# Kernel optimization log

Hardware: AMD Instinct MI355X
Metric: run time of the kernel (lower is better)

The kernel has to match this reference:

```python
import jax, jax.numpy as jnp
import numpy as np

N_NODES = 50000
N_EDGES = 800000
D_IN = 256
D_OUT = 256
N_REL = 8


def setup_inputs() -> dict:
    key = jax.random.key(0)
    k_x, k_ei, k_et, k_w = jax.random.split(key, 4)
    x = jax.random.normal(k_x, (N_NODES, D_IN), dtype=jnp.float32)
    edge_index = jax.random.randint(k_ei, (2, N_EDGES), 0, N_NODES, dtype=jnp.int32)
    edge_type = jax.random.randint(k_et, (N_EDGES,), 0, N_REL, dtype=jnp.int32)
    # xavier_uniform-style init for per-relation weights [R, I, O]
    limit = float(np.sqrt(6.0 / (D_IN + D_OUT)))
    weight = jax.random.uniform(k_w, (N_REL, D_IN, D_OUT), dtype=jnp.float32,
                                minval=-limit, maxval=limit)
    bias = jnp.zeros((D_OUT,), dtype=jnp.float32)
    return {"x": x, "edge_index": edge_index, "edge_type": edge_type,
            "weight": weight, "bias": bias}


def reference(x, edge_index, edge_type, weight, bias):
    # RGCN (block / per-relation weights):
    #   out[row] += x[col] @ weight[edge_type]
    # Vectorized: transform every node under every relation once (dense GEMM),
    # then gather the right (relation, col) slice per edge and scatter-add to row.
    num_nodes = x.shape[0]
    row, col = edge_index[0], edge_index[1]
    xt = jnp.einsum('ni,rio->rno', x, weight)          # [R, N, O]
    messages = xt[edge_type, col]                       # [E, O]
    out = jax.ops.segment_sum(messages, row, num_segments=num_nodes)  # [N, O]
    return jax.nn.relu(out + bias)
```

## Files before the change

### kernel.cpp

```cpp
#include <hip/hip_runtime.h>
#include <hip/hip_bf16.h>
#include <stdint.h>

typedef __attribute__((ext_vector_type(8))) short short8;
typedef __attribute__((ext_vector_type(4))) float f32x4;

#define D 256
#define NTY 4

static __device__ __forceinline__ float b2f(unsigned short u) {
  union { unsigned u; float f; } c; c.u = ((unsigned)u) << 16; return c.f;
}
static __device__ __forceinline__ unsigned short f2b(float f) {
  union { float f; unsigned u; } c; c.f = f;
  unsigned r = (c.u + 0x7FFFu + ((c.u >> 16) & 1u)) >> 16;
  return (unsigned short)r;
}

static __device__ __forceinline__ void gload16(const void* g, void* l) {
  __builtin_amdgcn_global_load_lds(
      (const __attribute__((address_space(1))) unsigned int*)g,
      (__attribute__((address_space(3))) unsigned int*)l, 16, 0, 0);
}

__global__ void k_cvt_x(const float* __restrict__ x, unsigned short* __restrict__ xb,
                        long n_elems, long pad_elems) {
  long i4 = (long)blockIdx.x * 256 + threadIdx.x;
  if (i4 * 4 >= pad_elems) return;
  ushort4 o;
  if (i4 * 4 < n_elems) {
    float4 v = ((const float4*)x)[i4];
    o.x = f2b(v.x); o.y = f2b(v.y); o.z = f2b(v.z); o.w = f2b(v.w);
  } else {
    o.x = 0; o.y = 0; o.z = 0; o.w = 0;
  }
  ((ushort4*)xb)[i4] = o;
}

__global__ void k_cvt_w(const float* __restrict__ w, unsigned short* __restrict__ wt,
                        int total) {
  int t = blockIdx.x * 256 + threadIdx.x;
  if (t >= total) return;
  int i = t & 255;
  int orow = t >> 8;
  int r = orow >> 8, o = orow & 255;
  wt[t] = f2b(w[((size_t)(r * 256 + i)) * 256 + o]);
}

__global__ __launch_bounds__(256) void k_gemm(const unsigned short* __restrict__ A,
                                              const unsigned short* __restrict__ B,
                                              unsigned short* __restrict__ C,
                                              int ldc) {
  __shared__ __align__(16) char lA[64 * 512];
  __shared__ __align__(16) char lB[128 * 128];
  const int t = threadIdx.x;
  const int lane = t & 63;
  const int wave = t >> 6;
  const int l15 = lane & 15, lhi = lane >> 4;
  const size_t tm = (size_t)blockIdx.x * 64;
  const int y0 = blockIdx.y * NTY;

#pragma unroll
  for (int it = 0; it < 8; ++it) {
    int s = it * 256 + t;
    int row = s >> 5, c = s & 31;
    gload16(A + (tm + row) * 256 + ((c ^ (row & 7)) * 8),
            lA + (it * 256 + wave * 64) * 16);
  }

  for (int y = y0; y < y0 + NTY; ++y) {
    const int tn = y * 128;
    f32x4 acc[4][2];
#pragma unroll
    for (int a = 0; a < 4; ++a)
#pragma unroll
      for (int b = 0; b < 2; ++b)
#pragma unroll
        for (int e = 0; e < 4; ++e) acc[a][b][e] = 0.f;

    for (int kt = 0; kt < 256; kt += 64) {
      __syncthreads();
#pragma unroll
      for (int it = 0; it < 4; ++it) {
        int s = it * 256 + t;
        int row = s >> 3, c = s & 7;
        gload16(B + (tn + row) * 256 + kt + ((c ^ (row & 7)) * 8),
                lB + (it * 256 + wave * 64) * 16);
      }
      __syncthreads();

      short8 af[4][2], bfv[2][2];
      const int ktc = kt >> 3;
#pragma unroll
      for (int mi = 0; mi < 4; ++mi) {
#pragma unroll
        for (int kk = 0; kk < 2; ++kk) {
          int R = mi * 16 + l15;
          int c = ktc + kk * 4 + lhi;
          af[mi][kk] = *(const short8*)(lA + R * 512 + ((c ^ (R & 7)) * 16));
        }
      }
#pragma unroll
      for (int ni = 0; ni < 2; ++ni) {
#pragma unroll
        for (int kk = 0; kk < 2; ++kk) {
          int R2 = wave * 32 + ni * 16 + l15;
          int c2 = kk * 4 + lhi;
          bfv[ni][kk] = *(const short8*)(lB + R2 * 128 + ((c2 ^ (R2 & 7)) * 16));
        }
      }
#pragma unroll
      for (int mi = 0; mi < 4; ++mi) {
#pragma unroll
        for (int ni = 0; ni < 2; ++ni) {
          acc[mi][ni] = __builtin_amdgcn_mfma_f32_16x16x32_bf16(af[mi][0], bfv[ni][0], acc[mi][ni], 0, 0, 0);
          acc[mi][ni] = __builtin_amdgcn_mfma_f32_16x16x32_bf16(af[mi][1], bfv[ni][1], acc[mi][ni], 0, 0, 0);
        }
      }
    }
#pragma unroll
    for (int mi = 0; mi < 4; ++mi) {
#pragma unroll
      for (int j = 0; j < 4; ++j) {
        size_t row = tm + mi * 16 + lhi * 4 + j;
        unsigned pk = (unsigned)f2b(acc[mi][0][j]) | ((unsigned)f2b(acc[mi][1][j]) << 16);
        *(unsigned*)(C + row * (size_t)ldc + tn + wave * 32 + l15 * 2) = pk;
      }
    }
  }
}

__global__ void k_zero(int* p, int n) {
  int i = blockIdx.x * 256 + threadIdx.x;
  if (i < n) p[i] = 0;
}
__global__ void k_deg(const int* __restrict__ ei, int* deg, int E) {
  int e = blockIdx.x * 256 + threadIdx.x;
  if (e < E) atomicAdd(&deg[ei[e]], 1);
}
__global__ void k_scan1(const int* __restrict__ deg, int* bsum, int n) {
  __shared__ int sm[256];
  int t = threadIdx.x, idx = blockIdx.x * 256 + t;
  sm[t] = idx < n ? deg[idx] : 0;
  __syncthreads();
  for (int off = 128; off; off >>= 1) {
    if (t < off) sm[t] += sm[t + off];
    __syncthreads();
  }
  if (t == 0) bsum[blockIdx.x] = sm[0];
}
__global__ void k_scan2(const int* __restrict__ bsum, int* boff, int* rowptr,
                        int nsc, int Nn) {
  __shared__ int sm[256];
  int t = threadIdx.x;
  int v = t < nsc ? bsum[t] : 0;
  sm[t] = v;
  __syncthreads();
  for (int off = 1; off < 256; off <<= 1) {
    int x = t >= off ? sm[t - off] : 0;
    __syncthreads();
    sm[t] += x;
    __syncthreads();
  }
  if (t < nsc) boff[t] = sm[t] - v;
  if (t == nsc - 1) rowptr[Nn] = sm[t];
}
__global__ void k_scan3(const int* __restrict__ deg, const int* __restrict__ boff,
                        int* rowptr, int* cursor, int n) {
  __shared__ int sm[256];
  int t = threadIdx.x, idx = blockIdx.x * 256 + t;
  int v = idx < n ? deg[idx] : 0;
  sm[t] = v;
  __syncthreads();
  for (int off = 1; off < 256; off <<= 1) {
    int x = t >= off ? sm[t - off] : 0;
    __syncthreads();
    sm[t] += x;
    __syncthreads();
  }
  if (idx < n) {
    int e = boff[blockIdx.x] + sm[t] - v;
    rowptr[idx] = e;
    cursor[idx] = e;
  }
}
__global__ void k_bin(const int* __restrict__ ei, const int* __restrict__ et,
                      int* cursor, unsigned* ect, int E) {
  int e = blockIdx.x * 256 + threadIdx.x;
  if (e >= E) return;
  int r = ei[e], c = ei[E + e], ty = et[e];
  int pos = atomicAdd(&cursor[r], 1);
  ect[pos] = (unsigned)c | ((unsigned)ty << 20);
}

__global__ __launch_bounds__(256) void k_gather(const unsigned* __restrict__ ect,
                                                const int* __restrict__ rowptr,
                                                const unsigned short* __restrict__ xt,
                                                const float* __restrict__ bias,
                                                float* __restrict__ out, int n, int ldxt) {
  __shared__ float sm[4][256];
  int lane = threadIdx.x & 63;
  int wid = threadIdx.x >> 6;
  int row = blockIdx.x * 4 + wid;
  if (row >= n) return;
  int s = rowptr[row], e = rowptr[row + 1];
  float a0 = 0.f, a1 = 0.f, a2 = 0.f, a3 = 0.f;
  unsigned myct = (s + lane < e) ? ect[s + lane] : 0u;
  int cnt = e - s;
  if (cnt > 64) cnt = 64;
  for (int i = 0; i < cnt; ++i) {
    unsigned ct = __shfl(myct, i);
    size_t base = (size_t)(ct & 0xFFFFFu) * ldxt + ((ct >> 20) << 8) + (lane << 2);
    ushort4 v = *(const ushort4*)(xt + base);
    a0 += b2f(v.x); a1 += b2f(v.y); a2 += b2f(v.z); a3 += b2f(v.w);
  }
  for (int i = s + 64; i < e; ++i) {
    unsigned ct = ect[i];
    size_t base = (size_t)(ct & 0xFFFFFu) * ldxt + ((ct >> 20) << 8) + (lane << 2);
    ushort4 v = *(const ushort4*)(xt + base);
    a0 += b2f(v.x); a1 += b2f(v.y); a2 += b2f(v.z); a3 += b2f(v.w);
  }
  int p0 = lane * 4;
  float av[4] = {a0, a1, a2, a3};
#pragma unroll
  for (int q = 0; q < 4; ++q) {
    int p8 = p0 + q;
    int o = (p8 & 224) | ((p8 & 1) << 4) | ((p8 & 31) >> 1);
    sm[wid][o] = av[q];
  }
  float4 v = *(const float4*)&sm[wid][lane * 4];
  float4 bb = ((const float4*)bias)[lane];
  float4 o;
  o.x = fmaxf(v.x + bb.x, 0.f);
  o.y = fmaxf(v.y + bb.y, 0.f);
  o.z = fmaxf(v.z + bb.z, 0.f);
  o.w = fmaxf(v.w + bb.w, 0.f);
  ((float4*)out)[(size_t)row * 64 + lane] = o;
}

extern "C" void kernel_launch(void* const* d_in, const int* in_sizes, int n_in,
                              void* d_out, int out_size, void* d_ws, size_t ws_size,
                              hipStream_t stream) {
  const float* x = (const float*)d_in[0];
  const int* ei = (const int*)d_in[1];
  const int* et = (const int*)d_in[2];
  const float* w = (const float*)d_in[3];
  const float* bias = (const float*)d_in[4];
  float* out = (float*)d_out;

  const int Nn = in_sizes[0] / D;
  const int E = in_sizes[2];
  const int R = in_sizes[3] / (D * D);
  const int Mpad = ((Nn + 63) / 64) * 64;
  const int NC = R * D;

  char* p = (char*)d_ws;
  auto alloc = [&](size_t bytes) -> char* {
    char* q = p;
    p += (bytes + 255) & ~(size_t)255;
    return q;
  };
  unsigned short* xt = (unsigned short*)alloc((size_t)Mpad * NC * 2);
  unsigned short* xb = (unsigned short*)alloc((size_t)Mpad * D * 2);
  unsigned short* wt = (unsigned short*)alloc((size_t)NC * D * 2);
  int* rowptr = (int*)alloc((size_t)(Nn + 1) * 4);
  int* cursor = (int*)alloc((size_t)Nn * 4);
  int* deg = (int*)alloc((size_t)Nn * 4);
  int* bsum = (int*)alloc(1024);
  int* boff = (int*)alloc(1024);
  unsigned* ect = (unsigned*)alloc((size_t)E * 4);

  const int nsc = (Nn + 255) / 256;

  hipLaunchKernelGGL(k_zero, dim3(nsc), dim3(256), 0, stream, deg, Nn);
  hipLaunchKernelGGL(k_deg, dim3((E + 255) / 256), dim3(256), 0, stream, ei, deg, E);
  hipLaunchKernelGGL(k_scan1, dim3(nsc), dim3(256), 0, stream, deg, bsum, Nn);
  hipLaunchKernelGGL(k_scan2, dim3(1), dim3(256), 0, stream, bsum, boff, rowptr, nsc, Nn);
  hipLaunchKernelGGL(k_scan3, dim3(nsc), dim3(256), 0, stream, deg, boff, rowptr, cursor, Nn);
  hipLaunchKernelGGL(k_bin, dim3((E + 255) / 256), dim3(256), 0, stream, ei, et, cursor, ect, E);

  hipLaunchKernelGGL(k_cvt_x, dim3(Mpad / 4), dim3(256), 0, stream, x, xb,
                     (long)Nn * D, (long)Mpad * D);
  hipLaunchKernelGGL(k_cvt_w, dim3((NC * D + 255) / 256), dim3(256), 0, stream, w, wt, NC * D);
  hipLaunchKernelGGL(k_gemm, dim3(Mpad / 64, NC / (128 * NTY)), dim3(256), 0, stream,
                     xb, wt, xt, NC);

  hipLaunchKernelGGL(k_gather, dim3((Nn + 3) / 4), dim3(256), 0, stream, ect, rowptr,
                     xt, bias, out, Nn, NC);
}
```

Before: 363.6 us.

## Merge setup kernels and widen gather loads to process two edges per wave

Merges the x and w conversion kernels into one launch and the two scan passes into one kernel, where every block redundantly scans the block sums. The zero kernel is replaced by hipMemsetAsync. The gather kernel now splits each wave into two half-waves that handle alternate edges with 16-byte loads, then combines the halves with a cross-lane shuffle. The aim is fewer launches and more memory parallelism in the gather, at the cost of redundant scan work per block.

Measured after the change: 356.2 us. 2.0% less time.

```diff
diff --git a/kernel.cpp b/kernel.cpp
--- a/kernel.cpp
+++ b/kernel.cpp
@@ -23,28 +23,27 @@
       (__attribute__((address_space(3))) unsigned int*)l, 16, 0, 0);
 }
 
-__global__ void k_cvt_x(const float* __restrict__ x, unsigned short* __restrict__ xb,
-                        long n_elems, long pad_elems) {
-  long i4 = (long)blockIdx.x * 256 + threadIdx.x;
-  if (i4 * 4 >= pad_elems) return;
-  ushort4 o;
-  if (i4 * 4 < n_elems) {
-    float4 v = ((const float4*)x)[i4];
-    o.x = f2b(v.x); o.y = f2b(v.y); o.z = f2b(v.z); o.w = f2b(v.w);
+__global__ void k_cvt_xw(const float* __restrict__ x, unsigned short* __restrict__ xb,
+                         long n_elems, long pad_elems, int xblocks,
+                         const float* __restrict__ w, unsigned short* __restrict__ wt) {
+  if (blockIdx.x < (unsigned)xblocks) {
+    long i4 = (long)blockIdx.x * 256 + threadIdx.x;
+    if (i4 * 4 >= pad_elems) return;
+    ushort4 o;
+    if (i4 * 4 < n_elems) {
+      float4 v = ((const float4*)x)[i4];
+      o.x = f2b(v.x); o.y = f2b(v.y); o.z = f2b(v.z); o.w = f2b(v.w);
+    } else {
+      o.x = 0; o.y = 0; o.z = 0; o.w = 0;
+    }
+    ((ushort4*)xb)[i4] = o;
   } else {
-    o.x = 0; o.y = 0; o.z = 0; o.w = 0;
-  }
-  ((ushort4*)xb)[i4] = o;
-}
-
-__global__ void k_cvt_w(const float* __restrict__ w, unsigned short* __restrict__ wt,
-                        int total) {
-  int t = blockIdx.x * 256 + threadIdx.x;
-  if (t >= total) return;
-  int i = t & 255;
-  int orow = t >> 8;
-  int r = orow >> 8, o = orow & 255;
-  wt[t] = f2b(w[((size_t)(r * 256 + i)) * 256 + o]);
+    int t = (blockIdx.x - xblocks) * 256 + threadIdx.x;
+    int i = t & 255;
+    int orow = t >> 8;
+    int r = orow >> 8, o = orow & 255;
+    wt[t] = f2b(w[((size_t)(r * 256 + i)) * 256 + o]);
+  }
 }
 
 __global__ __launch_bounds__(256) void k_gemm(const unsigned short* __restrict__ A,
@@ -130,10 +129,6 @@
   }
 }
 
-__global__ void k_zero(int* p, int n) {
-  int i = blockIdx.x * 256 + threadIdx.x;
-  if (i < n) p[i] = 0;
-}
 __global__ void k_deg(const int* __restrict__ ei, int* deg, int E) {
   int e = blockIdx.x * 256 + threadIdx.x;
   if (e < E) atomicAdd(&deg[ei[e]], 1);
@@ -149,26 +144,20 @@
   }
   if (t == 0) bsum[blockIdx.x] = sm[0];
 }
-__global__ void k_scan2(const int* __restrict__ bsum, int* boff, int* rowptr,
-                        int nsc, int Nn) {
+__global__ void k_scan23(const int* __restrict__ deg, const int* __restrict__ bsum,
+                         int* rowptr, int* cursor, int nsc, int n) {
+  __shared__ int sb[256];
   __shared__ int sm[256];
-  int t = threadIdx.x;
-  int v = t < nsc ? bsum[t] : 0;
-  sm[t] = v;
+  int t = threadIdx.x, idx = blockIdx.x * 256 + t;
+  int bv = t < nsc ? bsum[t] : 0;
+  sb[t] = bv;
   __syncthreads();
   for (int off = 1; off < 256; off <<= 1) {
-    int x = t >= off ? sm[t - off] : 0;
-    __syncthreads();
-    sm[t] += x;
-    __syncthreads();
-  }
-  if (t < nsc) boff[t] = sm[t] - v;
-  if (t == nsc - 1) rowptr[Nn] = sm[t];
-}
-__global__ void k_scan3(const int* __restrict__ deg, const int* __restrict__ boff,
-                        int* rowptr, int* cursor, int n) {
-  __shared__ int sm[256];
-  int t = threadIdx.x, idx = blockIdx.x * 256 + t;
+    int x = t >= off ? sb[t - off] : 0;
+    __syncthreads();
+    sb[t] += x;
+    __syncthreads();
+  }
   int v = idx < n ? deg[idx] : 0;
   sm[t] = v;
   __syncthreads();
@@ -178,11 +167,13 @@
     sm[t] += x;
     __syncthreads();
   }
+  int boff = sb[blockIdx.x] - bsum[blockIdx.x];
   if (idx < n) {
-    int e = boff[blockIdx.x] + sm[t] - v;
+    int e = boff + sm[t] - v;
     rowptr[idx] = e;
     cursor[idx] = e;
   }
+  if (blockIdx.x == 0 && t == 0) rowptr[n] = sb[nsc - 1];
 }
 __global__ void k_bin(const int* __restrict__ ei, const int* __restrict__ et,
                       int* cursor, unsigned* ect, int E) {
@@ -199,34 +190,46 @@
                                                 const float* __restrict__ bias,
                                                 float* __restrict__ out, int n, int ldxt) {
   __shared__ float sm[4][256];
-  int lane = threadIdx.x & 63;
-  int wid = threadIdx.x >> 6;
-  int row = blockIdx.x * 4 + wid;
+  const int lane = threadIdx.x & 63;
+  const int wid = threadIdx.x >> 6;
+  const int h = lane >> 5;
+  const int sl = lane & 31;
+  const int row = blockIdx.x * 4 + wid;
   if (row >= n) return;
-  int s = rowptr[row], e = rowptr[row + 1];
-  float a0 = 0.f, a1 = 0.f, a2 = 0.f, a3 = 0.f;
+  const int s = rowptr[row], e = rowptr[row + 1];
+  const int cnt = e - s;
+  float a[8] = {0.f, 0.f, 0.f, 0.f, 0.f, 0.f, 0.f, 0.f};
   unsigned myct = (s + lane < e) ? ect[s + lane] : 0u;
-  int cnt = e - s;
-  if (cnt > 64) cnt = 64;
-  for (int i = 0; i < cnt; ++i) {
-    unsigned ct = __shfl(myct, i);
-    size_t base = (size_t)(ct & 0xFFFFFu) * ldxt + ((ct >> 20) << 8) + (lane << 2);
-    ushort4 v = *(const ushort4*)(xt + base);
-    a0 += b2f(v.x); a1 += b2f(v.y); a2 += b2f(v.z); a3 += b2f(v.w);
-  }
-  for (int i = s + 64; i < e; ++i) {
-    unsigned ct = ect[i];
-    size_t base = (size_t)(ct & 0xFFFFFu) * ldxt + ((ct >> 20) << 8) + (lane << 2);
-    ushort4 v = *(const ushort4*)(xt + base);
-    a0 += b2f(v.x); a1 += b2f(v.y); a2 += b2f(v.z); a3 += b2f(v.w);
-  }
-  int p0 = lane * 4;
-  float av[4] = {a0, a1, a2, a3};
-#pragma unroll
-  for (int q = 0; q < 4; ++q) {
-    int p8 = p0 + q;
-    int o = (p8 & 224) | ((p8 & 1) << 4) | ((p8 & 31) >> 1);
-    sm[wid][o] = av[q];
+  int c1 = cnt > 64 ? 64 : cnt;
+  for (int i = 0; i < c1; i += 2) {
+    int j = i + h;
+    unsigned ct = __shfl(myct, j);
+    if (j < c1) {
+      size_t base = (size_t)(ct & 0xFFFFFu) * ldxt + ((ct >> 20) << 8) + (sl << 3);
+      short8 v = *(const short8*)(xt + base);
+#pragma unroll
+      for (int k = 0; k < 8; ++k) a[k] += b2f((unsigned short)v[k]);
+    }
+  }
+  for (int i = s + 64; i < e; i += 2) {
+    int j = i + h;
+    if (j < e) {
+      unsigned ct = ect[j];
+      size_t base = (size_t)(ct & 0xFFFFFu) * ldxt + ((ct >> 20) << 8) + (sl << 3);
+      short8 v = *(const short8*)(xt + base);
+#pragma unroll
+      for (int k = 0; k < 8; ++k) a[k] += b2f((unsigned short)v[k]);
+    }
+  }
+#pragma unroll
+  for (int k = 0; k < 8; ++k) a[k] += __shfl_xor(a[k], 32);
+  if (h == 0) {
+#pragma unroll
+    for (int k = 0; k < 8; ++k) {
+      int p8 = sl * 8 + k;
+      int o = (p8 & 224) | ((p8 & 1) << 4) | ((p8 & 31) >> 1);
+      sm[wid][o] = a[k];
+    }
   }
   float4 v = *(const float4*)&sm[wid][lane * 4];
   float4 bb = ((const float4*)bias)[lane];
@@ -267,21 +270,20 @@
   int* cursor = (int*)alloc((size_t)Nn * 4);
   int* deg = (int*)alloc((size_t)Nn * 4);
   int* bsum = (int*)alloc(1024);
-  int* boff = (int*)alloc(1024);
   unsigned* ect = (unsigned*)alloc((size_t)E * 4);
 
   const int nsc = (Nn + 255) / 256;
-
-  hipLaunchKernelGGL(k_zero, dim3(nsc), dim3(256), 0, stream, deg, Nn);
+  const int xblocks = Mpad / 4;
+
+  hipMemsetAsync(deg, 0, (size_t)Nn * 4, stream);
   hipLaunchKernelGGL(k_deg, dim3((E + 255) / 256), dim3(256), 0, stream, ei, deg, E);
   hipLaunchKernelGGL(k_scan1, dim3(nsc), dim3(256), 0, stream, deg, bsum, Nn);
-  hipLaunchKernelGGL(k_scan2, dim3(1), dim3(256), 0, stream, bsum, boff, rowptr, nsc, Nn);
-  hipLaunchKernelGGL(k_scan3, dim3(nsc), dim3(256), 0, stream, deg, boff, rowptr, cursor, Nn);
+  hipLaunchKernelGGL(k_scan23, dim3(nsc), dim3(256), 0, stream, deg, bsum,
+                     rowptr, cursor, nsc, Nn);
   hipLaunchKernelGGL(k_bin, dim3((E + 255) / 256), dim3(256), 0, stream, ei, et, cursor, ect, E);
 
-  hipLaunchKernelGGL(k_cvt_x, dim3(Mpad / 4), dim3(256), 0, stream, x, xb,
-                     (long)Nn * D, (long)Mpad * D);
-  hipLaunchKernelGGL(k_cvt_w, dim3((NC * D + 255) / 256), dim3(256), 0, stream, w, wt, NC * D);
+  hipLaunchKernelGGL(k_cvt_xw, dim3(xblocks + (NC * D) / 256), dim3(256), 0, stream,
+                     x, xb, (long)Nn * D, (long)Mpad * D, xblocks, w, wt);
   hipLaunchKernelGGL(k_gemm, dim3(Mpad / 64, NC / (128 * NTY)), dim3(256), 0, stream,
                      xb, wt, xt, NC);
 
```
